# Optimization experiments

Measured on AMD Instinct MI355X. Metric: run time of the kernel, lower is better.

## Reference

```python
import jax, jax.numpy as jnp
import numpy as np

K_STEPS = 12
NUM_NEG = 10
B, C, T = 2, 512, 4096


def setup_inputs() -> dict:
    key = jax.random.key(0)
    k0, k1, k2, k3, k4 = jax.random.split(key, 5)
    feat_enc = jax.random.normal(k0, (B, C, T), dtype=jnp.float32)
    feat_context = jax.random.normal(k1, (B, C, T), dtype=jnp.float32)
    W = jax.random.normal(k2, (C, C), dtype=jnp.float32) / np.float32(np.sqrt(C))
    b = jax.random.normal(k3, (C,), dtype=jnp.float32) * 0.01
    # stands in for torch.multinomial draws inside the k-loop: one [T, num_neg]
    # index set per step (values in [0, T))
    neg_idx = jax.random.randint(k4, (K_STEPS, T, NUM_NEG), 0, T, dtype=jnp.int32)
    return {"feat_enc": feat_enc, "feat_context": feat_context, "W": W, "b": b,
            "neg_idx": neg_idx}


def reference(feat_enc, feat_context, W, b, neg_idx):
    # linear over channel dim: (transpose -> Linear -> transpose) == einsum
    c = jnp.einsum('bct,dc->bdt', feat_context, W) + b[None, :, None]  # [B,C,T]
    # cont[b,t,s] = sum_c z[b,c,t] * c[b,c,s]  -> [B,T,T]
    cont = jnp.einsum('bct,bcs->bts', feat_enc, c)
    Bn, Tlen, _ = cont.shape
    total = jnp.zeros((), dtype=cont.dtype)
    for k in range(K_STEPS):
        # positives: diagonal offset=-k -> cont[b, i+k, i], length T-k
        pos = jnp.diagonal(cont, offset=-k, axis1=1, axis2=2)
        pos_loss = jnp.sum(jax.nn.log_sigmoid(pos))
        # torch: neg[b, s, r] = cont[b, s, neg_idx[k, r, s]] for s<num_neg
        idx = neg_idx[k].T  # [num_neg, T]
        idx_b = jnp.broadcast_to(idx[None], (Bn, NUM_NEG, Tlen))
        neg = jnp.take_along_axis(cont[:, :NUM_NEG, :], idx_b, axis=2)
        neg_loss = jnp.sum(jax.nn.log_sigmoid(-neg))
        total = total + pos_loss + NUM_NEG * neg_loss
    return total
```

## Files before the change

kernel.cpp:

```cpp
#include <hip/hip_runtime.h>
#include <hip/hip_bf16.h>

constexpr int KST  = 12;
constexpr int NN   = 10;
constexpr int B    = 2;
constexpr int C    = 512;
constexpr int T    = 4096;
constexpr int BAND = 12;
constexpr int NCH  = C / 32;

typedef float f32x4  __attribute__((ext_vector_type(4)));
typedef short bf16x8 __attribute__((ext_vector_type(8)));
typedef unsigned short u16x8 __attribute__((ext_vector_type(8)));

__device__ __forceinline__ float logsig(float x) {
    return fminf(x, 0.0f) - log1pf(expf(-fabsf(x)));
}
__device__ __forceinline__ unsigned short f2bf(float f) {
    union { float f; unsigned u; } v; v.f = f;
    unsigned r = v.u + 0x7fff + ((v.u >> 16) & 1);
    return (unsigned short)(r >> 16);
}

constexpr int PREP_TRANS_BLKS = 1024;
constexpr int PREP_GRID = PREP_TRANS_BLKS + (C * C) / (256 * 4);

__global__ __launch_bounds__(256) void prep_all(
    const float* __restrict__ fc, const float* __restrict__ enc,
    const float* __restrict__ W,
    unsigned short* __restrict__ fcp, unsigned short* __restrict__ encp,
    unsigned short* __restrict__ Wp, float* __restrict__ out)
{
    __shared__ float lt[64][65];
    const int bid = blockIdx.x;
    const int tid = threadIdx.x;

    if (bid < PREP_TRANS_BLKS) {
        #pragma unroll
        for (int r = 0; r < 2; ++r) {
            if (r) __syncthreads();
            const int j   = bid * 2 + r;
            const int z   = j >> 9;
            const int rem = j & 511;
            const int t0  = (rem & 63) * 64;
            const int c0  = (rem >> 6) * 64;
            const float* src = (z < 2 ? fc : enc) + (size_t)(z & 1) * C * T;
            unsigned short* dst =
                (z < 2 ? fcp : encp) + (size_t)(z & 1) * NCH * T * 32;

            const int tq = (tid & 15) * 4;
            const int cr = tid >> 4;
            #pragma unroll
            for (int p = 0; p < 4; ++p) {
                const int c_row = p * 16 + cr;
                const float4 v = *(const float4*)&src[(size_t)(c0 + c_row) * T + t0 + tq];
                lt[tq + 0][c_row] = v.x;
                lt[tq + 1][c_row] = v.y;
                lt[tq + 2][c_row] = v.z;
                lt[tq + 3][c_row] = v.w;
            }
            __syncthreads();

            const int t_row = tid >> 2;
            const int cq    = (tid & 3) * 16;
            u16x8 o0, o1;
            #pragma unroll
            for (int u = 0; u < 8; ++u) o0[u] = f2bf(lt[t_row][cq + u]);
            #pragma unroll
            for (int u = 0; u < 8; ++u) o1[u] = f2bf(lt[t_row][cq + 8 + u]);
            const int cg = c0 + cq;
            const int ks = cg >> 5;
            const int j0 = cg & 31;
            unsigned short* dp = dst + ((size_t)ks * T + t0 + t_row) * 32 + j0;
            *(u16x8*)dp       = o0;
            *(u16x8*)(dp + 8) = o1;
        }
    } else {
        if (bid == PREP_TRANS_BLKS && tid == 0) out[0] = 0.0f;
        const int idx = ((bid - PREP_TRANS_BLKS) * 256 + tid) * 4;
        const int d = idx >> 9;
        const int k = idx & 511;
        const float4 v = *(const float4*)&W[idx];
        ushort4 o;
        o.x = f2bf(v.x); o.y = f2bf(v.y); o.z = f2bf(v.z); o.w = f2bf(v.w);
        *(ushort4*)&Wp[((size_t)(k >> 5) * C + d) * 32 + (k & 31)] = o;
    }
}

__global__ __launch_bounds__(256) void cgemm(
    const unsigned short* __restrict__ Wp, const unsigned short* __restrict__ fcp,
    const float* __restrict__ bias, unsigned short* __restrict__ cpk)
{
    const int bid   = blockIdx.x;
    const int panel = bid & 127;
    const int d0    = (bid >> 7) * 64;
    const int t0    = (panel & 63) * 64;
    const int b     = panel >> 6;

    __shared__ unsigned short c_lds[64][68];

    const int lane = threadIdx.x & 63;
    const int w    = threadIdx.x >> 6;
    const int wt   = (w >> 1) * 32;
    const int wd   = (w & 1) * 32;
    const int l15  = lane & 15;
    const int l4   = lane >> 4;

    const unsigned short* fcpb = fcp + (size_t)b * NCH * T * 32;
    const unsigned short* An = fcpb + (size_t)(t0 + wt + l15) * 32 + l4 * 8;
    const unsigned short* Bn = Wp   + (size_t)(d0 + wd + l15) * 32 + l4 * 8;

    f32x4 acc[2][2] = {};
    #pragma unroll 4
    for (int ks = 0; ks < NCH; ++ks) {
        const size_t ao = (size_t)ks * T * 32;
        const size_t bo = (size_t)ks * C * 32;
        const bf16x8 a0 = *(const bf16x8*)(An + ao);
        const bf16x8 a1 = *(const bf16x8*)(An + ao + 16 * 32);
        const bf16x8 b0 = *(const bf16x8*)(Bn + bo);
        const bf16x8 b1 = *(const bf16x8*)(Bn + bo + 16 * 32);
        acc[0][0] = __builtin_amdgcn_mfma_f32_16x16x32_bf16(a0, b0, acc[0][0], 0, 0, 0);
        acc[0][1] = __builtin_amdgcn_mfma_f32_16x16x32_bf16(a0, b1, acc[0][1], 0, 0, 0);
        acc[1][0] = __builtin_amdgcn_mfma_f32_16x16x32_bf16(a1, b0, acc[1][0], 0, 0, 0);
        acc[1][1] = __builtin_amdgcn_mfma_f32_16x16x32_bf16(a1, b1, acc[1][1], 0, 0, 0);
    }

    #pragma unroll
    for (int j = 0; j < 2; ++j) {
        const int dcol = wd + j * 16 + l15;
        const float bv = bias[d0 + dcol];
        #pragma unroll
        for (int i = 0; i < 2; ++i) {
            const int trow = wt + i * 16 + l4 * 4;
            #pragma unroll
            for (int r = 0; r < 4; ++r)
                c_lds[trow + r][dcol] = f2bf(acc[i][j][r] + bv);
        }
    }
    __syncthreads();

    {
        const int t     = threadIdx.x >> 2;
        const int piece = threadIdx.x & 3;
        const int ks    = (d0 >> 5) + (piece >> 1);
        const int inner = (piece & 1) * 16;
        const u16x8 o0 = *(const u16x8*)&c_lds[t][piece * 16];
        const u16x8 o1 = *(const u16x8*)&c_lds[t][piece * 16 + 8];
        unsigned short* dp = cpk + (size_t)b * NCH * T * 32
                           + ((size_t)ks * T + t0 + t) * 32 + inner;
        *(u16x8*)dp       = o0;
        *(u16x8*)(dp + 8) = o1;
    }
}

__global__ __launch_bounds__(512) void band_kernel(
    const unsigned short* __restrict__ encp, const unsigned short* __restrict__ cpk,
    float* __restrict__ negls, float* __restrict__ out)
{
    const int b  = blockIdx.y;
    const int n0 = blockIdx.x * 32;
    __shared__ float posred[8];

    const int tid  = threadIdx.x;
    const int lane = tid & 63;
    const int w    = tid >> 6;
    const int l15  = lane & 15;
    const int l4   = lane >> 4;

    const unsigned short* encpb = encp + (size_t)b * NCH * T * 32;
    const unsigned short* cpkb  = cpk  + (size_t)b * NCH * T * 32;

    const int i2 = w >> 1;
    const int j2 = w & 1;
    const int rg = i2 * 16 + l15;
    int ti;
    if (rg < 44) { ti = n0 + rg; ti = ti < T ? ti : T - 1; }
    else if (rg < 54) ti = rg - 44;
    else ti = 0;
    const unsigned short* A2p = encpb + (size_t)ti * 32 + l4 * 8;
    const unsigned short* B2p = cpkb + (size_t)(n0 + j2 * 16 + l15) * 32 + l4 * 8;

    f32x4 dacc = {};
    #pragma unroll 4
    for (int ks = 0; ks < NCH; ++ks) {
        const size_t o = (size_t)ks * T * 32;
        const bf16x8 a2 = *(const bf16x8*)(A2p + o);
        const bf16x8 b2 = *(const bf16x8*)(B2p + o);
        dacc = __builtin_amdgcn_mfma_f32_16x16x32_bf16(a2, b2, dacc, 0, 0, 0);
    }

    float pos = 0.0f;
    const int colr = j2 * 16 + l15;
    const int scol = n0 + colr;
    #pragma unroll
    for (int r = 0; r < 4; ++r) {
        const int row = i2 * 16 + l4 * 4 + r;
        const float vv = dacc[r];
        if (row < 44) {
            const int k = row - colr;
            if (k >= 0 && k < BAND && scol + k < T) pos += logsig(vv);
        } else if (row < 54) {
            negls[((size_t)b * NN + (row - 44)) * T + scol] = logsig(-vv);
        }
    }
    #pragma unroll
    for (int off = 32; off > 0; off >>= 1) pos += __shfl_down(pos, off, 64);
    if (lane == 0) posred[w] = pos;
    __syncthreads();
    if (tid == 0) {
        float tsum = 0.0f;
        #pragma unroll
        for (int q = 0; q < 8; ++q) tsum += posred[q];
        atomicAdd(out, tsum);
    }
}

__global__ __launch_bounds__(256) void gather_kernel(
    const int4* __restrict__ nidx4, const float* __restrict__ negls,
    float* __restrict__ out)
{
    constexpr int TOTAL4 = KST * T * NN / 4;
    float local = 0.0f;
    for (int i4 = blockIdx.x * 256 + threadIdx.x; i4 < TOTAL4; i4 += 120 * 256) {
        const int4 vv = nidx4[i4];
        const int base = i4 * 4;
        const int idxs[4] = {vv.x, vv.y, vv.z, vv.w};
        #pragma unroll
        for (int e = 0; e < 4; ++e) {
            const int n = (base + e) % NN;
            local += negls[(size_t)n * T + idxs[e]]
                   + negls[(size_t)(NN + n) * T + idxs[e]];
        }
    }
    #pragma unroll
    for (int off = 32; off > 0; off >>= 1) local += __shfl_down(local, off, 64);
    __shared__ float wsum[4];
    if ((threadIdx.x & 63) == 0) wsum[threadIdx.x >> 6] = local;
    __syncthreads();
    if (threadIdx.x == 0)
        atomicAdd(out, (float)NN * (wsum[0] + wsum[1] + wsum[2] + wsum[3]));
}

extern "C" void kernel_launch(void* const* d_in, const int* in_sizes, int n_in,
                              void* d_out, int out_size, void* d_ws, size_t ws_size,
                              hipStream_t stream)
{
    const float* enc  = (const float*)d_in[0];
    const float* fc   = (const float*)d_in[1];
    const float* W    = (const float*)d_in[2];
    const float* bias = (const float*)d_in[3];
    const int4*  nidx4 = (const int4*)d_in[4];
    float* out = (float*)d_out;

    unsigned short* fcp  = (unsigned short*)d_ws;
    unsigned short* encp = fcp  + (size_t)B * NCH * T * 32;
    unsigned short* Wp   = encp + (size_t)B * NCH * T * 32;
    unsigned short* cpk  = Wp   + (size_t)C * C;
    float* negls = (float*)(cpk + (size_t)B * NCH * T * 32);

    prep_all<<<PREP_GRID, 256, 0, stream>>>(fc, enc, W, fcp, encp, Wp, out);
    cgemm<<<1024, 256, 0, stream>>>(Wp, fcp, bias, cpk);
    band_kernel<<<dim3(T / 32, B), 512, 0, stream>>>(encp, cpk, negls, out);
    gather_kernel<<<120, 256, 0, stream>>>(nidx4, negls, out);
}
```

Before: 52.33 us.

## Split band kernel K-reduction across wave pairs with LDS combine

The band kernel now covers 16 columns per block instead of 32 and launches twice as many blocks. Each pair of waves splits the 16 channel chunks into two halves of 8, and the partial MFMA accumulators are summed through shared memory before the log-sigmoid and reduction step. The aim is more parallelism and a shorter serial MFMA/load chain per wave. In exchange, the enc rows (44 overlapping band rows) are reloaded by more blocks, and the kernel adds an LDS round-trip and an extra barrier.

```diff
diff --git a/kernel.cpp b/kernel.cpp
--- a/kernel.cpp
+++ b/kernel.cpp
@@ -158,61 +158,71 @@
     float* __restrict__ negls, float* __restrict__ out)
 {
     const int b  = blockIdx.y;
-    const int n0 = blockIdx.x * 32;
-    __shared__ float posred[8];
+    const int n0 = blockIdx.x * 16;
+
+    __shared__ float red[4][64][4];
+    __shared__ float posred[4];
 
     const int tid  = threadIdx.x;
     const int lane = tid & 63;
     const int w    = tid >> 6;
+    const int i2   = w >> 1;
+    const int h    = w & 1;
     const int l15  = lane & 15;
     const int l4   = lane >> 4;
 
     const unsigned short* encpb = encp + (size_t)b * NCH * T * 32;
     const unsigned short* cpkb  = cpk  + (size_t)b * NCH * T * 32;
 
-    const int i2 = w >> 1;
-    const int j2 = w & 1;
     const int rg = i2 * 16 + l15;
     int ti;
     if (rg < 44) { ti = n0 + rg; ti = ti < T ? ti : T - 1; }
     else if (rg < 54) ti = rg - 44;
     else ti = 0;
-    const unsigned short* A2p = encpb + (size_t)ti * 32 + l4 * 8;
-    const unsigned short* B2p = cpkb + (size_t)(n0 + j2 * 16 + l15) * 32 + l4 * 8;
+    const unsigned short* A2p = encpb + (size_t)ti * 32 + l4 * 8
+                              + (size_t)(h * 8) * T * 32;
+    const unsigned short* B2p = cpkb + (size_t)(n0 + l15) * 32 + l4 * 8
+                              + (size_t)(h * 8) * T * 32;
 
     f32x4 dacc = {};
-    #pragma unroll 4
-    for (int ks = 0; ks < NCH; ++ks) {
+    #pragma unroll
+    for (int ks = 0; ks < 8; ++ks) {
         const size_t o = (size_t)ks * T * 32;
         const bf16x8 a2 = *(const bf16x8*)(A2p + o);
         const bf16x8 b2 = *(const bf16x8*)(B2p + o);
         dacc = __builtin_amdgcn_mfma_f32_16x16x32_bf16(a2, b2, dacc, 0, 0, 0);
     }
 
-    float pos = 0.0f;
-    const int colr = j2 * 16 + l15;
-    const int scol = n0 + colr;
-    #pragma unroll
-    for (int r = 0; r < 4; ++r) {
-        const int row = i2 * 16 + l4 * 4 + r;
-        const float vv = dacc[r];
-        if (row < 44) {
-            const int k = row - colr;
-            if (k >= 0 && k < BAND && scol + k < T) pos += logsig(vv);
-        } else if (row < 54) {
-            negls[((size_t)b * NN + (row - 44)) * T + scol] = logsig(-vv);
-        }
-    }
-    #pragma unroll
-    for (int off = 32; off > 0; off >>= 1) pos += __shfl_down(pos, off, 64);
-    if (lane == 0) posred[w] = pos;
-    __syncthreads();
-    if (tid == 0) {
-        float tsum = 0.0f;
-        #pragma unroll
-        for (int q = 0; q < 8; ++q) tsum += posred[q];
-        atomicAdd(out, tsum);
-    }
+    if (h == 1) {
+        #pragma unroll
+        for (int r = 0; r < 4; ++r) red[i2][lane][r] = dacc[r];
+    }
+    __syncthreads();
+
+    if (h == 0) {
+        #pragma unroll
+        for (int r = 0; r < 4; ++r) dacc[r] += red[i2][lane][r];
+
+        float pos = 0.0f;
+        const int scol = n0 + l15;
+        #pragma unroll
+        for (int r = 0; r < 4; ++r) {
+            const int row = i2 * 16 + l4 * 4 + r;
+            const float vv = dacc[r];
+            if (row < 44) {
+                const int k = row - l15;
+                if (k >= 0 && k < BAND && scol + k < T) pos += logsig(vv);
+            } else if (row < 54) {
+                negls[((size_t)b * NN + (row - 44)) * T + scol] = logsig(-vv);
+            }
+        }
+        #pragma unroll
+        for (int off = 32; off > 0; off >>= 1) pos += __shfl_down(pos, off, 64);
+        if (lane == 0) posred[i2] = pos;
+    }
+    __syncthreads();
+    if (tid == 0)
+        atomicAdd(out, posred[0] + posred[1] + posred[2] + posred[3]);
 }
 
 __global__ __launch_bounds__(256) void gather_kernel(
@@ -260,6 +270,6 @@
 
     prep_all<<<PREP_GRID, 256, 0, stream>>>(fc, enc, W, fcp, encp, Wp, out);
     cgemm<<<1024, 256, 0, stream>>>(Wp, fcp, bias, cpk);
-    band_kernel<<<dim3(T / 32, B), 512, 0, stream>>>(encp, cpk, negls, out);
+    band_kernel<<<dim3(T / 16, B), 512, 0, stream>>>(encp, cpk, negls, out);
     gather_kernel<<<120, 256, 0, stream>>>(nidx4, negls, out);
 }
```

Measured after the change: 54.73 us. +4.6%, slower.

## Stage cgemm operand tiles through double-buffered LDS with register prefetch

Applied to the files above, without the earlier changes.

Replaces the direct per-wave global loads of A and B fragments in the c-projection GEMM with cooperative loads into double-buffered shared-memory tiles (padded stride 40), prefetching two k-steps ahead into registers. The aim is to cut redundant global traffic, since each wave previously loaded overlapping fragments, and to hide load latency behind the MFMAs. It adds one barrier per k-step and extra LDS usage, which may limit occupancy or add sync overhead in this short 16-step loop.

```diff
diff --git a/kernel.cpp b/kernel.cpp
--- a/kernel.cpp
+++ b/kernel.cpp
@@ -97,28 +97,53 @@
     const int t0    = (panel & 63) * 64;
     const int b     = panel >> 6;
 
+    __shared__ unsigned short A_lds[2][64 * 40];
+    __shared__ unsigned short B_lds[2][64 * 40];
     __shared__ unsigned short c_lds[64][68];
 
-    const int lane = threadIdx.x & 63;
-    const int w    = threadIdx.x >> 6;
+    const int tid  = threadIdx.x;
+    const int lane = tid & 63;
+    const int w    = tid >> 6;
     const int wt   = (w >> 1) * 32;
     const int wd   = (w & 1) * 32;
     const int l15  = lane & 15;
     const int l4   = lane >> 4;
 
-    const unsigned short* fcpb = fcp + (size_t)b * NCH * T * 32;
-    const unsigned short* An = fcpb + (size_t)(t0 + wt + l15) * 32 + l4 * 8;
-    const unsigned short* Bn = Wp   + (size_t)(d0 + wd + l15) * 32 + l4 * 8;
+    const unsigned short* Ag = fcp + (size_t)b * NCH * T * 32
+                             + (size_t)t0 * 32 + tid * 8;
+    const unsigned short* Bg = Wp + (size_t)d0 * 32 + tid * 8;
+
+    const int sdst = (tid >> 2) * 40 + (tid & 3) * 8;
+
+    bf16x8 ar = *(const bf16x8*)(Ag);
+    bf16x8 br = *(const bf16x8*)(Bg);
+    *(bf16x8*)&A_lds[0][sdst] = ar;
+    *(bf16x8*)&B_lds[0][sdst] = br;
+    ar = *(const bf16x8*)(Ag + (size_t)1 * T * 32);
+    br = *(const bf16x8*)(Bg + (size_t)1 * C * 32);
+
+    const int fa0 = (wt + l15) * 40 + l4 * 8;
+    const int fa1 = (wt + 16 + l15) * 40 + l4 * 8;
+    const int fb0 = (wd + l15) * 40 + l4 * 8;
+    const int fb1 = (wd + 16 + l15) * 40 + l4 * 8;
 
     f32x4 acc[2][2] = {};
     #pragma unroll 4
     for (int ks = 0; ks < NCH; ++ks) {
-        const size_t ao = (size_t)ks * T * 32;
-        const size_t bo = (size_t)ks * C * 32;
-        const bf16x8 a0 = *(const bf16x8*)(An + ao);
-        const bf16x8 a1 = *(const bf16x8*)(An + ao + 16 * 32);
-        const bf16x8 b0 = *(const bf16x8*)(Bn + bo);
-        const bf16x8 b1 = *(const bf16x8*)(Bn + bo + 16 * 32);
+        __syncthreads();
+        const int cur = ks & 1;
+        const bf16x8 a0 = *(const bf16x8*)&A_lds[cur][fa0];
+        const bf16x8 a1 = *(const bf16x8*)&A_lds[cur][fa1];
+        const bf16x8 b0 = *(const bf16x8*)&B_lds[cur][fb0];
+        const bf16x8 b1 = *(const bf16x8*)&B_lds[cur][fb1];
+        if (ks + 1 < NCH) {
+            *(bf16x8*)&A_lds[cur ^ 1][sdst] = ar;
+            *(bf16x8*)&B_lds[cur ^ 1][sdst] = br;
+        }
+        if (ks + 2 < NCH) {
+            ar = *(const bf16x8*)(Ag + (size_t)(ks + 2) * T * 32);
+            br = *(const bf16x8*)(Bg + (size_t)(ks + 2) * C * 32);
+        }
         acc[0][0] = __builtin_amdgcn_mfma_f32_16x16x32_bf16(a0, b0, acc[0][0], 0, 0, 0);
         acc[0][1] = __builtin_amdgcn_mfma_f32_16x16x32_bf16(a0, b1, acc[0][1], 0, 0, 0);
         acc[1][0] = __builtin_amdgcn_mfma_f32_16x16x32_bf16(a1, b0, acc[1][0], 0, 0, 0);
@@ -140,8 +165,8 @@
     __syncthreads();
 
     {
-        const int t     = threadIdx.x >> 2;
-        const int piece = threadIdx.x & 3;
+        const int t     = tid >> 2;
+        const int piece = tid & 3;
         const int ks    = (d0 >> 5) + (piece >> 1);
         const int inner = (piece & 1) * 16;
         const u16x8 o0 = *(const u16x8*)&c_lds[t][piece * 16];
```

New measurement: 46.29 us, median of 2. 11.5% less time.

## Retile c-GEMM to 128x128 blocks with double-buffered LDS staging

Applied to the files above, without the earlier changes.

The c = W·feat_context GEMM moves from 64x64 tiles, where each wave loads its fragments straight from global memory, to 128x128 tiles. Each tile stages A and B through double-buffered shared memory, with register prefetch two k-steps ahead. Each wave now computes a 64x64 sub-tile with 16 MFMAs per k-step, which raises operand reuse and cuts redundant global loads. The grid shrinks from 1024 to 256 blocks, which lowers parallelism on a many-CU GPU and adds a barrier per k-step.

```diff
diff --git a/kernel.cpp b/kernel.cpp
--- a/kernel.cpp
+++ b/kernel.cpp
@@ -91,65 +91,109 @@
     const unsigned short* __restrict__ Wp, const unsigned short* __restrict__ fcp,
     const float* __restrict__ bias, unsigned short* __restrict__ cpk)
 {
-    const int bid   = blockIdx.x;
-    const int panel = bid & 127;
-    const int d0    = (bid >> 7) * 64;
-    const int t0    = (panel & 63) * 64;
-    const int b     = panel >> 6;
-
-    __shared__ unsigned short c_lds[64][68];
-
-    const int lane = threadIdx.x & 63;
-    const int w    = threadIdx.x >> 6;
-    const int wt   = (w >> 1) * 32;
-    const int wd   = (w & 1) * 32;
+    const int bid = blockIdx.x;
+    const int d0  = (bid >> 6) * 128;
+    const int rem = bid & 63;
+    const int t0  = (rem >> 1) * 128;
+    const int b   = rem & 1;
+
+    __shared__ unsigned short smem[4][128 * 40];
+
+    const int tid  = threadIdx.x;
+    const int lane = tid & 63;
+    const int w    = tid >> 6;
+    const int wt   = (w >> 1) * 64;
+    const int wd   = (w & 1) * 64;
     const int l15  = lane & 15;
     const int l4   = lane >> 4;
 
-    const unsigned short* fcpb = fcp + (size_t)b * NCH * T * 32;
-    const unsigned short* An = fcpb + (size_t)(t0 + wt + l15) * 32 + l4 * 8;
-    const unsigned short* Bn = Wp   + (size_t)(d0 + wd + l15) * 32 + l4 * 8;
-
-    f32x4 acc[2][2] = {};
-    #pragma unroll 4
+    const unsigned short* Ag = fcp + (size_t)b * NCH * T * 32 + (size_t)t0 * 32;
+    const unsigned short* Bg = Wp + (size_t)d0 * 32;
+
+    const int srow  = tid >> 2;
+    const int scol  = (tid & 3) * 8;
+    const int sdst0 = srow * 40 + scol;
+    const int sdst1 = (srow + 64) * 40 + scol;
+    const int goff0 = tid * 8;
+    const int goff1 = tid * 8 + 2048;
+
+    bf16x8 ar0 = *(const bf16x8*)(Ag + goff0);
+    bf16x8 ar1 = *(const bf16x8*)(Ag + goff1);
+    bf16x8 br0 = *(const bf16x8*)(Bg + goff0);
+    bf16x8 br1 = *(const bf16x8*)(Bg + goff1);
+    *(bf16x8*)&smem[0][sdst0] = ar0;
+    *(bf16x8*)&smem[0][sdst1] = ar1;
+    *(bf16x8*)&smem[1][sdst0] = br0;
+    *(bf16x8*)&smem[1][sdst1] = br1;
+    ar0 = *(const bf16x8*)(Ag + (size_t)1 * T * 32 + goff0);
+    ar1 = *(const bf16x8*)(Ag + (size_t)1 * T * 32 + goff1);
+    br0 = *(const bf16x8*)(Bg + (size_t)1 * C * 32 + goff0);
+    br1 = *(const bf16x8*)(Bg + (size_t)1 * C * 32 + goff1);
+
+    f32x4 acc[4][4] = {};
+    #pragma unroll 2
     for (int ks = 0; ks < NCH; ++ks) {
-        const size_t ao = (size_t)ks * T * 32;
-        const size_t bo = (size_t)ks * C * 32;
-        const bf16x8 a0 = *(const bf16x8*)(An + ao);
-        const bf16x8 a1 = *(const bf16x8*)(An + ao + 16 * 32);
-        const bf16x8 b0 = *(const bf16x8*)(Bn + bo);
-        const bf16x8 b1 = *(const bf16x8*)(Bn + bo + 16 * 32);
-        acc[0][0] = __builtin_amdgcn_mfma_f32_16x16x32_bf16(a0, b0, acc[0][0], 0, 0, 0);
-        acc[0][1] = __builtin_amdgcn_mfma_f32_16x16x32_bf16(a0, b1, acc[0][1], 0, 0, 0);
-        acc[1][0] = __builtin_amdgcn_mfma_f32_16x16x32_bf16(a1, b0, acc[1][0], 0, 0, 0);
-        acc[1][1] = __builtin_amdgcn_mfma_f32_16x16x32_bf16(a1, b1, acc[1][1], 0, 0, 0);
-    }
-
+        __syncthreads();
+        const int cur = ks & 1;
+        bf16x8 afr[4], bfr[4];
+        #pragma unroll
+        for (int i = 0; i < 4; ++i)
+            afr[i] = *(const bf16x8*)&smem[cur * 2][(wt + i * 16 + l15) * 40 + l4 * 8];
+        #pragma unroll
+        for (int j = 0; j < 4; ++j)
+            bfr[j] = *(const bf16x8*)&smem[cur * 2 + 1][(wd + j * 16 + l15) * 40 + l4 * 8];
+
+        if (ks + 1 < NCH) {
+            *(bf16x8*)&smem[(cur ^ 1) * 2][sdst0]     = ar0;
+            *(bf16x8*)&smem[(cur ^ 1) * 2][sdst1]     = ar1;
+            *(bf16x8*)&smem[(cur ^ 1) * 2 + 1][sdst0] = br0;
+            *(bf16x8*)&smem[(cur ^ 1) * 2 + 1][sdst1] = br1;
+        }
+        if (ks + 2 < NCH) {
+            ar0 = *(const bf16x8*)(Ag + (size_t)(ks + 2) * T * 32 + goff0);
+            ar1 = *(const bf16x8*)(Ag + (size_t)(ks + 2) * T * 32 + goff1);
+            br0 = *(const bf16x8*)(Bg + (size_t)(ks + 2) * C * 32 + goff0);
+            br1 = *(const bf16x8*)(Bg + (size_t)(ks + 2) * C * 32 + goff1);
+        }
+        #pragma unroll
+        for (int i = 0; i < 4; ++i)
+            #pragma unroll
+            for (int j = 0; j < 4; ++j)
+                acc[i][j] = __builtin_amdgcn_mfma_f32_16x16x32_bf16(
+                    afr[i], bfr[j], acc[i][j], 0, 0, 0);
+    }
+    __syncthreads();
+
+    unsigned short* c_lds = &smem[0][0];
     #pragma unroll
-    for (int j = 0; j < 2; ++j) {
+    for (int j = 0; j < 4; ++j) {
         const int dcol = wd + j * 16 + l15;
         const float bv = bias[d0 + dcol];
         #pragma unroll
-        for (int i = 0; i < 2; ++i) {
+        for (int i = 0; i < 4; ++i) {
             const int trow = wt + i * 16 + l4 * 4;
             #pragma unroll
             for (int r = 0; r < 4; ++r)
-                c_lds[trow + r][dcol] = f2bf(acc[i][j][r] + bv);
+                c_lds[(trow + r) * 136 + dcol] = f2bf(acc[i][j][r] + bv);
         }
     }
     __syncthreads();
 
     {
-        const int t     = threadIdx.x >> 2;
-        const int piece = threadIdx.x & 3;
-        const int ks    = (d0 >> 5) + (piece >> 1);
-        const int inner = (piece & 1) * 16;
-        const u16x8 o0 = *(const u16x8*)&c_lds[t][piece * 16];
-        const u16x8 o1 = *(const u16x8*)&c_lds[t][piece * 16 + 8];
-        unsigned short* dp = cpk + (size_t)b * NCH * T * 32
-                           + ((size_t)ks * T + t0 + t) * 32 + inner;
-        *(u16x8*)dp       = o0;
-        *(u16x8*)(dp + 8) = o1;
+        const int row  = tid >> 1;
+        const int half = (tid & 1) * 64;
+        #pragma unroll
+        for (int q = 0; q < 2; ++q) {
+            const int dloc = half + q * 32;
+            const int ks2  = (d0 + dloc) >> 5;
+            unsigned short* dp = cpk + (size_t)b * NCH * T * 32
+                               + ((size_t)ks2 * T + t0 + row) * 32;
+            const unsigned short* sp = &c_lds[row * 136 + dloc];
+            *(u16x8*)(dp)      = *(const u16x8*)(sp);
+            *(u16x8*)(dp + 8)  = *(const u16x8*)(sp + 8);
+            *(u16x8*)(dp + 16) = *(const u16x8*)(sp + 16);
+            *(u16x8*)(dp + 24) = *(const u16x8*)(sp + 24);
+        }
     }
 }
 
@@ -259,7 +303,7 @@
     float* negls = (float*)(cpk + (size_t)B * NCH * T * 32);
 
     prep_all<<<PREP_GRID, 256, 0, stream>>>(fc, enc, W, fcp, encp, Wp, out);
-    cgemm<<<1024, 256, 0, stream>>>(Wp, fcp, bias, cpk);
+    cgemm<<<256, 256, 0, stream>>>(Wp, fcp, bias, cpk);
     band_kernel<<<dim3(T / 32, B), 512, 0, stream>>>(encp, cpk, negls, out);
     gather_kernel<<<120, 256, 0, stream>>>(nidx4, negls, out);
 }
```

New measurement: 47.09 us. 1.11x faster.
